# Optimization experiments

Hardware: AMD Instinct MI355X
Metric: run time of the kernel (lower is better)

The kernel has to match this reference:

```python
import jax, jax.numpy as jnp
import numpy as np

# Static config (matches init_kwargs)
B, H, W, C = 16, 64, 64, 512
HEADS, WS, SHIFT = 16, 8, 4
N = WS * WS                      # tokens per window = 64
NW = (H // WS) * (W // WS)       # windows per image = 64
HID = 4 * C                      # MLP hidden = 2048
HEAD_DIM = C // HEADS
SCALE = HEAD_DIM ** -0.5
EPS = 1e-5


def _layer_norm(x, w, b):
    m = jnp.mean(x, axis=-1, keepdims=True)
    v = jnp.mean((x - m) ** 2, axis=-1, keepdims=True)
    return (x - m) / jnp.sqrt(v + EPS) * w + b


def _rel_pos_idx():
    coords = np.stack(np.meshgrid(np.arange(WS), np.arange(WS), indexing='ij')).reshape(2, -1)
    rel = coords[:, :, None] - coords[:, None, :]          # (2, N, N)
    rel = rel.transpose(1, 2, 0)                           # (N, N, 2)
    rel[:, :, 0] += WS - 1
    rel[:, :, 1] += WS - 1
    rel[:, :, 0] *= 2 * WS - 1
    return rel.sum(-1)                                     # (N, N) int


def _attn_mask():
    img = np.zeros((H, W), dtype=np.float32)
    sls = (slice(0, -WS), slice(-WS, -SHIFT), slice(-SHIFT, None))
    cnt = 0
    for hs in sls:
        for ws_ in sls:
            img[hs, ws_] = cnt
            cnt += 1
    # window partition (H,W) -> (NW, N)
    mw = img.reshape(H // WS, WS, W // WS, WS).transpose(0, 2, 1, 3).reshape(-1, N)
    diff = mw[:, None, :] - mw[:, :, None]                 # (NW, N, N)
    return np.where(diff != 0, -100.0, 0.0).astype(np.float32)


def setup_inputs() -> dict:
    key = jax.random.key(0)
    ks = jax.random.split(key, 8)
    s = 0.02
    return {
        'x': jax.random.normal(ks[0], (B, H * W, C), jnp.float32),
        'qkv_w': jax.random.normal(ks[1], (3 * C, C), jnp.float32) * s,
        'qkv_b': jnp.zeros((3 * C,), jnp.float32),
        'proj_w': jax.random.normal(ks[2], (C, C), jnp.float32) * s,
        'proj_b': jnp.zeros((C,), jnp.float32),
        'norm1_w': jnp.ones((C,), jnp.float32),
        'norm1_b': jnp.zeros((C,), jnp.float32),
        'norm2_w': jnp.ones((C,), jnp.float32),
        'norm2_b': jnp.zeros((C,), jnp.float32),
        'fc1_w': jax.random.normal(ks[3], (HID, C), jnp.float32) * s,
        'fc1_b': jnp.zeros((HID,), jnp.float32),
        'fc2_w': jax.random.normal(ks[4], (C, HID), jnp.float32) * s,
        'fc2_b': jnp.zeros((C,), jnp.float32),
        'rel_bias_table': jax.random.normal(ks[5], ((2 * WS - 1) ** 2, HEADS), jnp.float32) * s,
        'rel_pos_idx': jnp.asarray(_rel_pos_idx(), jnp.int32),
        'attn_mask': jnp.asarray(_attn_mask(), jnp.float32),
    }


def _swin_block(x, qkv_w, qkv_b, proj_w, proj_b, norm1_w, norm1_b,
                norm2_w, norm2_b, fc1_w, fc1_b, fc2_w, fc2_b,
                rel_bias_table, rel_pos_idx, attn_mask):
    Bx = x.shape[0]
    shortcut = x
    h = _layer_norm(x, norm1_w, norm1_b).reshape(Bx, H, W, C)
    h = jnp.roll(h, (-SHIFT, -SHIFT), axis=(1, 2))
    # window partition -> (B*NW, N, C)
    h = h.reshape(Bx, H // WS, WS, W // WS, WS, C).transpose(0, 1, 3, 2, 4, 5)
    h = h.reshape(Bx * NW, N, C)
    # qkv projection
    qkv = h @ qkv_w.T + qkv_b                               # (B_, N, 3C)
    qkv = qkv.reshape(Bx * NW, N, 3, HEADS, HEAD_DIM).transpose(2, 0, 3, 1, 4)
    q, k, v = qkv[0], qkv[1], qkv[2]                        # (B_, heads, N, hd)
    attn = jnp.einsum('bhnd,bhmd->bhnm', q, k) * SCALE      # (B_, heads, N, N)
    rp_bias = rel_bias_table[rel_pos_idx]                   # (N, N, heads)
    attn = attn + rp_bias.transpose(2, 0, 1)[None]
    # shift mask (per window)
    attn = attn.reshape(Bx, NW, HEADS, N, N) + attn_mask[None, :, None]
    attn = jax.nn.softmax(attn.reshape(Bx * NW, HEADS, N, N), axis=-1)
    o = jnp.einsum('bhnm,bhmd->bhnd', attn, v)              # (B_, heads, N, hd)
    o = o.transpose(0, 2, 1, 3).reshape(Bx * NW, N, C)
    o = o @ proj_w.T + proj_b
    # window reverse -> (B, H, W, C)
    o = o.reshape(Bx, H // WS, W // WS, WS, WS, C).transpose(0, 1, 3, 2, 4, 5)
    o = o.reshape(Bx, H, W, C)
    o = jnp.roll(o, (SHIFT, SHIFT), axis=(1, 2))
    x = shortcut + o.reshape(Bx, H * W, C)
    # MLP
    h2 = _layer_norm(x, norm2_w, norm2_b)
    h2 = jax.nn.gelu(h2 @ fc1_w.T + fc1_b, approximate=False)
    return x + (h2 @ fc2_w.T + fc2_b)


def reference(x, qkv_w, qkv_b, proj_w, proj_b, norm1_w, norm1_b,
              norm2_w, norm2_b, fc1_w, fc1_b, fc2_w, fc2_b,
              rel_bias_table, rel_pos_idx, attn_mask):
    return _swin_block(x, qkv_w, qkv_b, proj_w, proj_b, norm1_w, norm1_b,
                       norm2_w, norm2_b, fc1_w, fc1_b, fc2_w, fc2_b,
                       rel_bias_table, rel_pos_idx, attn_mask)
```

## Files before the change

kernel.cpp:

```cpp
#include <hip/hip_runtime.h>
#include <hip/hip_bf16.h>

typedef __attribute__((ext_vector_type(8))) short short8;
typedef __attribute__((ext_vector_type(4))) float f32x4;

__device__ __forceinline__ short f2bfbits(float f) {
  union { __hip_bfloat16 h; short s; } cvt;
  cvt.h = __float2bfloat16(f);
  return cvt.s;
}
__device__ __forceinline__ float bfbits2f(short bits) {
  union { unsigned int u; float f; } cvt;
  cvt.u = ((unsigned int)(unsigned short)bits) << 16;
  return cvt.f;
}

__device__ __forceinline__ void gl_lds16(const short* g, short* l) {
  __builtin_amdgcn_global_load_lds(
      (__attribute__((address_space(1))) void*)(g),
      (__attribute__((address_space(3))) void*)(l), 16, 0, 0);
}

__global__ __launch_bounds__(256)
void f2bf(const float* __restrict__ s, short* __restrict__ d, int n) {
  const int i = (blockIdx.x * 256 + threadIdx.x) * 4;
  if (i >= n) return;
  float4 v = *(const float4*)(s + i);
  short o[4] = {f2bfbits(v.x), f2bfbits(v.y), f2bfbits(v.z), f2bfbits(v.w)};
  *(uint2*)(d + i) = *(const uint2*)o;
}

__global__ __launch_bounds__(256)
void bm_build(const float* __restrict__ table, const int* __restrict__ idx,
              const float* __restrict__ mask, short* __restrict__ bm) {
  const int wi = blockIdx.x, hh = blockIdx.y;
  const int n = threadIdx.x & 63;
  const int m0 = (threadIdx.x >> 6) * 16;
#pragma unroll
  for (int mm = 0; mm < 16; mm++) {
    const int m = m0 + mm;
    const float t = table[idx[m * 64 + n] * 16 + hh];
    const float mk = mask[wi * 4096 + m * 64 + n];
    bm[((long)(wi * 16 + hh) * 64 + m) * 64 + n] = f2bfbits(t + mk);
  }
}

__global__ __launch_bounds__(256)
void ln1_win(const float* __restrict__ x, const float* __restrict__ w,
             const float* __restrict__ b, short* __restrict__ h) {
  const int lane = threadIdx.x & 63;
  const int wv = threadIdx.x >> 6;
  const int t = blockIdx.x * 4 + wv;
  const int n = t & 63, wiB = t >> 6;
  const int wi = wiB & 63, bb = wiB >> 6;
  const int sr = (((wi >> 3) << 3) + (n >> 3) + 4) & 63;
  const int sc = (((wi & 7) << 3) + (n & 7) + 4) & 63;
  const float* xp = x + ((long)bb * 4096 + sr * 64 + sc) * 512 + lane * 8;
  float4 u0 = *(const float4*)(xp);
  float4 u1 = *(const float4*)(xp + 4);
  float v[8] = {u0.x, u0.y, u0.z, u0.w, u1.x, u1.y, u1.z, u1.w};
  float s = 0.f;
#pragma unroll
  for (int j = 0; j < 8; j++) s += v[j];
#pragma unroll
  for (int o = 1; o < 64; o <<= 1) s += __shfl_xor(s, o, 64);
  const float mean = s * (1.0f / 512.0f);
  float q = 0.f;
#pragma unroll
  for (int j = 0; j < 8; j++) { float d = v[j] - mean; q += d * d; }
#pragma unroll
  for (int o = 1; o < 64; o <<= 1) q += __shfl_xor(q, o, 64);
  const float rstd = rsqrtf(q * (1.0f / 512.0f) + 1e-5f);
  float4 w0 = *(const float4*)(w + lane * 8);
  float4 w1 = *(const float4*)(w + lane * 8 + 4);
  float4 b0 = *(const float4*)(b + lane * 8);
  float4 b1 = *(const float4*)(b + lane * 8 + 4);
  const float wv8[8] = {w0.x, w0.y, w0.z, w0.w, w1.x, w1.y, w1.z, w1.w};
  const float bv8[8] = {b0.x, b0.y, b0.z, b0.w, b1.x, b1.y, b1.z, b1.w};
  short outs[8];
#pragma unroll
  for (int j = 0; j < 8; j++)
    outs[j] = f2bfbits((v[j] - mean) * rstd * wv8[j] + bv8[j]);
  *(uint4*)(h + (long)t * 512 + lane * 8) = *(const uint4*)outs;
}

__global__ __launch_bounds__(256)
void ln2_id(const float* __restrict__ x2, const float* __restrict__ w,
            const float* __restrict__ b, short* __restrict__ out) {
  const int lane = threadIdx.x & 63;
  const int wv = threadIdx.x >> 6;
  const long t = blockIdx.x * 4 + wv;
  const float* xp = x2 + t * 512 + lane * 8;
  float4 u0 = *(const float4*)(xp);
  float4 u1 = *(const float4*)(xp + 4);
  float v[8] = {u0.x, u0.y, u0.z, u0.w, u1.x, u1.y, u1.z, u1.w};
  float s = 0.f;
#pragma unroll
  for (int j = 0; j < 8; j++) s += v[j];
#pragma unroll
  for (int o = 1; o < 64; o <<= 1) s += __shfl_xor(s, o, 64);
  const float mean = s * (1.0f / 512.0f);
  float q = 0.f;
#pragma unroll
  for (int j = 0; j < 8; j++) { float d = v[j] - mean; q += d * d; }
#pragma unroll
  for (int o = 1; o < 64; o <<= 1) q += __shfl_xor(q, o, 64);
  const float rstd = rsqrtf(q * (1.0f / 512.0f) + 1e-5f);
  float4 w0 = *(const float4*)(w + lane * 8);
  float4 w1 = *(const float4*)(w + lane * 8 + 4);
  float4 b0 = *(const float4*)(b + lane * 8);
  float4 b1 = *(const float4*)(b + lane * 8 + 4);
  const float wv8[8] = {w0.x, w0.y, w0.z, w0.w, w1.x, w1.y, w1.z, w1.w};
  const float bv8[8] = {b0.x, b0.y, b0.z, b0.w, b1.x, b1.y, b1.z, b1.w};
  short outs[8];
#pragma unroll
  for (int j = 0; j < 8; j++)
    outs[j] = f2bfbits((v[j] - mean) * rstd * wv8[j] + bv8[j]);
  *(uint4*)(out + t * 512 + lane * 8) = *(const uint4*)outs;
}

template <int MODE, int K, int GN>
__global__ __launch_bounds__(256, 2)
void gemm128(const short* __restrict__ A, const short* __restrict__ Bw,
             const float* __restrict__ bias, const float* __restrict__ aux,
             void* __restrict__ outv, short* __restrict__ out2) {
  __shared__ short lds[32768];
  constexpr int NT = K / 64;
  const int tid = threadIdx.x;
  const int lane = tid & 63, wave = tid >> 6;
  const int l15 = lane & 15, quad = lane >> 4;
  const int wr = wave >> 1, wc = wave & 1;

  const int nwg = gridDim.x;
  const int chunk = nwg >> 3;
  const int wg = (blockIdx.x & 7) * chunk + (blockIdx.x >> 3);
  const int row0 = (wg / GN) * 128;
  const int col0 = (wg % GN) * 128;

  const int srow = lane >> 3;
  const int scol = ((lane & 7) ^ srow) * 8;
  const short* Ag = A + (long)(row0 + wave * 32 + srow) * K + scol;
  const short* Bg = Bw + (long)(col0 + wave * 32 + srow) * K + scol;
  short* ldsAw = lds + wave * 2048;
  short* ldsBw = lds + 16384 + wave * 2048;

  const int g0 = (quad ^ (l15 & 7)) * 8;
  const int g1 = ((quad ^ 4) ^ (l15 & 7)) * 8;
  const int aB0 = (wr * 64 + l15) * 64 + g0;
  const int aB1 = (wr * 64 + l15) * 64 + g1;
  const int bB0 = 16384 + (wc * 64 + l15) * 64 + g0;
  const int bB1 = 16384 + (wc * 64 + l15) * 64 + g1;

  f32x4 acc[4][4];
#pragma unroll
  for (int m = 0; m < 4; m++)
#pragma unroll
    for (int n = 0; n < 4; n++) acc[m][n] = (f32x4){0.f, 0.f, 0.f, 0.f};

#define STAGE(cOff, kt)                                               \
  {                                                                   \
    const short* a_ = Ag + (kt) * 64;                                 \
    const short* b_ = Bg + (kt) * 64;                                 \
    _Pragma("unroll") for (int i_ = 0; i_ < 4; i_++) {                \
      gl_lds16(a_ + (long)i_ * 8 * K, ldsAw + (cOff) + i_ * 512);     \
      gl_lds16(b_ + (long)i_ * 8 * K, ldsBw + (cOff) + i_ * 512);     \
    }                                                                 \
  }

  STAGE(0, 0);
  STAGE(8192, 1);
  asm volatile("s_waitcnt vmcnt(8)" ::: "memory");
  __builtin_amdgcn_s_barrier();

  for (int t = 0; t < NT; ++t) {
    const int c = (t & 1) << 13;
    const short* pa0 = lds + c + aB0;
    const short* pa1 = lds + c + aB1;
    const short* pb0 = lds + c + bB0;
    const short* pb1 = lds + c + bB1;
    short8 A0[4], A1[4], B0[4], B1[4];

#pragma unroll
    for (int n = 0; n < 4; n++) B0[n] = *(const short8*)(pb0 + n * 1024);
#pragma unroll
    for (int m = 0; m < 4; m++) A0[m] = *(const short8*)(pa0 + m * 1024);
    asm volatile("" ::: "memory");
    __builtin_amdgcn_s_barrier();
    __builtin_amdgcn_s_setprio(1);
#pragma unroll
    for (int m = 0; m < 4; m++)
#pragma unroll
      for (int n = 0; n < 4; n++)
        acc[m][n] = __builtin_amdgcn_mfma_f32_16x16x32_bf16(A0[m], B0[n], acc[m][n], 0, 0, 0);
    __builtin_amdgcn_s_setprio(0);
    __builtin_amdgcn_s_barrier();

#pragma unroll
    for (int m = 0; m < 4; m++) A1[m] = *(const short8*)(pa1 + m * 1024);
#pragma unroll
    for (int n = 0; n < 4; n++) B1[n] = *(const short8*)(pb1 + n * 1024);
    asm volatile("s_waitcnt lgkmcnt(0)" ::: "memory");
    __builtin_amdgcn_s_barrier();
    if (t + 2 < NT) STAGE(c, t + 2);
    __builtin_amdgcn_s_setprio(1);
#pragma unroll
    for (int m = 0; m < 4; m++)
#pragma unroll
      for (int n = 0; n < 4; n++)
        acc[m][n] = __builtin_amdgcn_mfma_f32_16x16x32_bf16(A1[m], B1[n], acc[m][n], 0, 0, 0);
    __builtin_amdgcn_s_setprio(0);
    if (t + 2 < NT) {
      asm volatile("s_waitcnt vmcnt(8)" ::: "memory");
    } else if (t + 1 < NT) {
      asm volatile("s_waitcnt vmcnt(0)" ::: "memory");
    }
    __builtin_amdgcn_s_barrier();
  }
#undef STAGE

  const int rW = row0 + wr * 64;
  const int cW = col0 + wc * 64;
  if constexpr (MODE == 0) {
    if (col0 >= 1024) {
#pragma unroll
      for (int m = 0; m < 4; m++) {
        const int rbase = rW + m * 16 + quad * 4;
        const int w_ = rbase >> 6, tokb = rbase & 63;
#pragma unroll
        for (int n = 0; n < 4; n++) {
          const int col = cW + n * 16 + l15;
          const float bv = bias[col];
          const int cg = col - 1024;
          const int head = cg >> 5, d = cg & 31;
          short pk[4];
#pragma unroll
          for (int r = 0; r < 4; r++) pk[r] = f2bfbits(acc[m][n][r] + bv);
          *(uint2*)(out2 + ((long)(w_ * 16 + head) * 32 + d) * 64 + tokb) =
              *(const uint2*)pk;
        }
      }
    } else {
#pragma unroll
      for (int m = 0; m < 4; m++)
#pragma unroll
        for (int n = 0; n < 4; n++) {
          const int col = cW + n * 16 + l15;
          const float bv = bias[col];
#pragma unroll
          for (int r = 0; r < 4; r++) {
            const int row = rW + m * 16 + quad * 4 + r;
            ((short*)outv)[(long)row * 1024 + col] = f2bfbits(acc[m][n][r] + bv);
          }
        }
    }
  } else {
#pragma unroll
    for (int m = 0; m < 4; m++)
#pragma unroll
      for (int n = 0; n < 4; n++) {
        const int col = cW + n * 16 + l15;
        const float bv = bias[col];
#pragma unroll
        for (int r = 0; r < 4; r++) {
          const int row = rW + m * 16 + quad * 4 + r;
          float v = acc[m][n][r] + bv;
          if constexpr (MODE == 1) {
            const int n_ = row & 63, wiB = row >> 6;
            const int wi = wiB & 63, bb = wiB >> 6;
            const int p = (((wi >> 3) << 3) + (n_ >> 3) + 4) & 63;
            const int qq = (((wi & 7) << 3) + (n_ & 7) + 4) & 63;
            const long dst = ((long)bb * 4096 + p * 64 + qq) * 512 + col;
            ((float*)outv)[dst] = v + aux[dst];
          } else if constexpr (MODE == 2) {
            const float g = 0.5f * v * (1.0f + erff(v * 0.70710678118654752f));
            ((short*)outv)[(long)row * (GN * 128) + col] = f2bfbits(g);
          } else {
            const long ix = (long)row * (GN * 128) + col;
            ((float*)outv)[ix] = v + aux[ix];
          }
        }
      }
  }
}

__global__ __launch_bounds__(256)
void attn(const short* __restrict__ qk, const short* __restrict__ vT,
          const short* __restrict__ bm, short* __restrict__ o) {
  __shared__ short P[4][64 * 72];
  const int lane = threadIdx.x & 63, wave = threadIdx.x >> 6;
  const int l15 = lane & 15, quad = lane >> 4;
  const int w = blockIdx.x;
  const int hh = blockIdx.y * 4 + wave;
  const int wi = w & 63;
  const short* base = qk + (long)w * 64 * 1024;

  short8 qf[4], kf[4];
#pragma unroll
  for (int mt = 0; mt < 4; mt++) {
    const int tq = mt * 16 + l15;
    qf[mt] = *(const short8*)(base + tq * 1024 + hh * 32 + quad * 8);
    kf[mt] = *(const short8*)(base + tq * 1024 + 512 + hh * 32 + quad * 8);
  }
  f32x4 S[4][4];
#pragma unroll
  for (int i = 0; i < 4; i++)
#pragma unroll
    for (int j = 0; j < 4; j++) S[i][j] = (f32x4){0.f, 0.f, 0.f, 0.f};
#pragma unroll
  for (int mt = 0; mt < 4; mt++)
#pragma unroll
    for (int nt = 0; nt < 4; nt++)
      S[mt][nt] = __builtin_amdgcn_mfma_f32_16x16x32_bf16(qf[mt], kf[nt], S[mt][nt], 0, 0, 0);

  short* pw = P[wave];
  const short* bmp = bm + (long)(wi * 16 + hh) * 4096;
  const float scale = 0.17677669529663687f;
#pragma unroll
  for (int mt = 0; mt < 4; mt++) {
#pragma unroll
    for (int reg = 0; reg < 4; reg++) {
      const int m = mt * 16 + quad * 4 + reg;
      float vals[4];
#pragma unroll
      for (int nt = 0; nt < 4; nt++)
        vals[nt] = S[mt][nt][reg] * scale + bfbits2f(bmp[m * 64 + nt * 16 + l15]);
      float mx = fmaxf(fmaxf(vals[0], vals[1]), fmaxf(vals[2], vals[3]));
#pragma unroll
      for (int o_ = 1; o_ < 16; o_ <<= 1) mx = fmaxf(mx, __shfl_xor(mx, o_, 64));
      float e[4], sum = 0.f;
#pragma unroll
      for (int nt = 0; nt < 4; nt++) { e[nt] = __expf(vals[nt] - mx); sum += e[nt]; }
#pragma unroll
      for (int o_ = 1; o_ < 16; o_ <<= 1) sum += __shfl_xor(sum, o_, 64);
      const float inv = 1.0f / sum;
#pragma unroll
      for (int nt = 0; nt < 4; nt++)
        pw[m * 72 + nt * 16 + l15] = f2bfbits(e[nt] * inv);
    }
  }

  const short* vbase = vT + (long)(w * 16 + hh) * 2048;
  f32x4 O[4][2];
#pragma unroll
  for (int i = 0; i < 4; i++)
#pragma unroll
    for (int j = 0; j < 2; j++) O[i][j] = (f32x4){0.f, 0.f, 0.f, 0.f};
#pragma unroll
  for (int ks = 0; ks < 2; ks++) {
    short8 vf[2];
#pragma unroll
    for (int nt = 0; nt < 2; nt++)
      vf[nt] = *(const short8*)(vbase + (nt * 16 + l15) * 64 + ks * 32 + quad * 8);
#pragma unroll
    for (int mt = 0; mt < 4; mt++) {
      short8 pf = *(const short8*)(pw + (mt * 16 + l15) * 72 + ks * 32 + quad * 8);
#pragma unroll
      for (int nt = 0; nt < 2; nt++)
        O[mt][nt] = __builtin_amdgcn_mfma_f32_16x16x32_bf16(pf, vf[nt], O[mt][nt], 0, 0, 0);
    }
  }
#pragma unroll
  for (int mt = 0; mt < 4; mt++)
#pragma unroll
    for (int nt = 0; nt < 2; nt++)
#pragma unroll
      for (int reg = 0; reg < 4; reg++) {
        const int t = mt * 16 + quad * 4 + reg;
        const int d = nt * 16 + l15;
        o[((long)w * 64 + t) * 512 + hh * 32 + d] = f2bfbits(O[mt][nt][reg]);
      }
}

extern "C" void kernel_launch(void* const* d_in, const int* in_sizes, int n_in,
                              void* d_out, int out_size, void* d_ws, size_t ws_size,
                              hipStream_t stream) {
  const float* x      = (const float*)d_in[0];
  const float* qkv_w  = (const float*)d_in[1];
  const float* qkv_b  = (const float*)d_in[2];
  const float* proj_w = (const float*)d_in[3];
  const float* proj_b = (const float*)d_in[4];
  const float* n1w    = (const float*)d_in[5];
  const float* n1b    = (const float*)d_in[6];
  const float* n2w    = (const float*)d_in[7];
  const float* n2b    = (const float*)d_in[8];
  const float* fc1_w  = (const float*)d_in[9];
  const float* fc1_b  = (const float*)d_in[10];
  const float* fc2_w  = (const float*)d_in[11];
  const float* fc2_b  = (const float*)d_in[12];
  const float* table  = (const float*)d_in[13];
  const int*   idx    = (const int*)d_in[14];
  const float* mask   = (const float*)d_in[15];

  char* ws = (char*)d_ws;
  const long MB = 1048576L;
  short* wq  = (short*)(ws);
  short* wp  = wq + 786432;
  short* w1  = wp + 262144;
  short* w2  = w1 + 1048576;
  short* bm  = (short*)(ws + 8 * MB);
  short* h   = (short*)(ws + 17 * MB);
  short* o   = h;
  short* xn2 = h;
  short* qk  = (short*)(ws + 81 * MB);
  short* h2c = qk;
  short* vT  = (short*)(ws + 209 * MB);
  float* out = (float*)d_out;

  f2bf<<<768, 256, 0, stream>>>(qkv_w, wq, 786432);
  f2bf<<<256, 256, 0, stream>>>(proj_w, wp, 262144);
  f2bf<<<1024, 256, 0, stream>>>(fc1_w, w1, 1048576);
  f2bf<<<1024, 256, 0, stream>>>(fc2_w, w2, 1048576);
  bm_build<<<dim3(64, 16), 256, 0, stream>>>(table, idx, mask, bm);

  ln1_win<<<16384, 256, 0, stream>>>(x, n1w, n1b, h);
  gemm128<0, 512, 12><<<6144, 256, 0, stream>>>(h, wq, qkv_b, nullptr, qk, vT);
  attn<<<dim3(1024, 4), 256, 0, stream>>>(qk, vT, bm, o);
  gemm128<1, 512, 4><<<2048, 256, 0, stream>>>(o, wp, proj_b, x, out, nullptr);
  ln2_id<<<16384, 256, 0, stream>>>(out, n2w, n2b, xn2);
  for (int c = 0; c < 2; c++) {
    const long ro = (long)c * 32768;
    gemm128<2, 512, 16><<<4096, 256, 0, stream>>>(
        xn2 + ro * 512, w1, fc1_b, nullptr, h2c, nullptr);
    gemm128<3, 2048, 4><<<1024, 256, 0, stream>>>(
        h2c, w2, fc2_b, out + ro * 512, out + ro * 512, nullptr);
  }
}
```

Baseline: 991.1 us.

## Halve GEMM K-tile to 32 and raise occupancy to four blocks per CU

Shrinks the per-stage K tile of the bf16 MFMA GEMM from 64 to 32, which halves the shared-memory buffer. That lets launch bounds request four workgroups per CU instead of two. The global-to-LDS staging layout is rewritten into 8-row blocks grouped by k, so each fragment read is a contiguous 128-byte run and the XOR swizzle is no longer needed. The inner loop becomes a single MFMA phase per tile. The goal is better latency hiding through higher occupancy, paid for with twice as many loop iterations and barriers per unit of work and a tighter register budget.

```diff
diff --git a/kernel.cpp b/kernel.cpp
--- a/kernel.cpp
+++ b/kernel.cpp
@@ -120,12 +120,12 @@
 }
 
 template <int MODE, int K, int GN>
-__global__ __launch_bounds__(256, 2)
+__global__ __launch_bounds__(256, 4)
 void gemm128(const short* __restrict__ A, const short* __restrict__ Bw,
              const float* __restrict__ bias, const float* __restrict__ aux,
              void* __restrict__ outv, short* __restrict__ out2) {
-  __shared__ short lds[32768];
-  constexpr int NT = K / 64;
+  __shared__ short lds[16384];
+  constexpr int NT = K / 32;
   const int tid = threadIdx.x;
   const int lane = tid & 63, wave = tid >> 6;
   const int l15 = lane & 15, quad = lane >> 4;
@@ -137,19 +137,15 @@
   const int row0 = (wg / GN) * 128;
   const int col0 = (wg % GN) * 128;
 
-  const int srow = lane >> 3;
-  const int scol = ((lane & 7) ^ srow) * 8;
-  const short* Ag = A + (long)(row0 + wave * 32 + srow) * K + scol;
-  const short* Bg = Bw + (long)(col0 + wave * 32 + srow) * K + scol;
-  short* ldsAw = lds + wave * 2048;
-  short* ldsBw = lds + 16384 + wave * 2048;
-
-  const int g0 = (quad ^ (l15 & 7)) * 8;
-  const int g1 = ((quad ^ 4) ^ (l15 & 7)) * 8;
-  const int aB0 = (wr * 64 + l15) * 64 + g0;
-  const int aB1 = (wr * 64 + l15) * 64 + g1;
-  const int bB0 = 16384 + (wc * 64 + l15) * 64 + g0;
-  const int bB1 = 16384 + (wc * 64 + l15) * 64 + g1;
+  const int srow = ((lane >> 5) << 3) + (lane & 7);
+  const int skg = (lane >> 3) & 3;
+  const short* Ag = A + (long)(row0 + wave * 32 + srow) * K + skg * 8;
+  const short* Bg = Bw + (long)(col0 + wave * 32 + srow) * K + skg * 8;
+  short* ldsAw = lds + wave * 1024;
+  short* ldsBw = lds + 4096 + wave * 1024;
+
+  const int aOff = (wr * 8 + (l15 >> 3)) * 256 + quad * 64 + (l15 & 7) * 8;
+  const int bOff = 4096 + (wc * 8 + (l15 >> 3)) * 256 + quad * 64 + (l15 & 7) * 8;
 
   f32x4 acc[4][4];
 #pragma unroll
@@ -159,46 +155,26 @@
 
 #define STAGE(cOff, kt)                                               \
   {                                                                   \
-    const short* a_ = Ag + (kt) * 64;                                 \
-    const short* b_ = Bg + (kt) * 64;                                 \
-    _Pragma("unroll") for (int i_ = 0; i_ < 4; i_++) {                \
-      gl_lds16(a_ + (long)i_ * 8 * K, ldsAw + (cOff) + i_ * 512);     \
-      gl_lds16(b_ + (long)i_ * 8 * K, ldsBw + (cOff) + i_ * 512);     \
+    const short* a_ = Ag + (kt) * 32;                                 \
+    const short* b_ = Bg + (kt) * 32;                                 \
+    _Pragma("unroll") for (int i_ = 0; i_ < 2; i_++) {                \
+      gl_lds16(a_ + (long)i_ * 16 * K, ldsAw + (cOff) + i_ * 512);    \
+      gl_lds16(b_ + (long)i_ * 16 * K, ldsBw + (cOff) + i_ * 512);    \
     }                                                                 \
   }
 
   STAGE(0, 0);
   STAGE(8192, 1);
-  asm volatile("s_waitcnt vmcnt(8)" ::: "memory");
+  asm volatile("s_waitcnt vmcnt(4)" ::: "memory");
   __builtin_amdgcn_s_barrier();
 
   for (int t = 0; t < NT; ++t) {
     const int c = (t & 1) << 13;
-    const short* pa0 = lds + c + aB0;
-    const short* pa1 = lds + c + aB1;
-    const short* pb0 = lds + c + bB0;
-    const short* pb1 = lds + c + bB1;
-    short8 A0[4], A1[4], B0[4], B1[4];
-
-#pragma unroll
-    for (int n = 0; n < 4; n++) B0[n] = *(const short8*)(pb0 + n * 1024);
-#pragma unroll
-    for (int m = 0; m < 4; m++) A0[m] = *(const short8*)(pa0 + m * 1024);
-    asm volatile("" ::: "memory");
-    __builtin_amdgcn_s_barrier();
-    __builtin_amdgcn_s_setprio(1);
-#pragma unroll
-    for (int m = 0; m < 4; m++)
-#pragma unroll
-      for (int n = 0; n < 4; n++)
-        acc[m][n] = __builtin_amdgcn_mfma_f32_16x16x32_bf16(A0[m], B0[n], acc[m][n], 0, 0, 0);
-    __builtin_amdgcn_s_setprio(0);
-    __builtin_amdgcn_s_barrier();
-
-#pragma unroll
-    for (int m = 0; m < 4; m++) A1[m] = *(const short8*)(pa1 + m * 1024);
-#pragma unroll
-    for (int n = 0; n < 4; n++) B1[n] = *(const short8*)(pb1 + n * 1024);
+    short8 Af[4], Bf[4];
+#pragma unroll
+    for (int n = 0; n < 4; n++) Bf[n] = *(const short8*)(lds + c + bOff + n * 512);
+#pragma unroll
+    for (int m = 0; m < 4; m++) Af[m] = *(const short8*)(lds + c + aOff + m * 512);
     asm volatile("s_waitcnt lgkmcnt(0)" ::: "memory");
     __builtin_amdgcn_s_barrier();
     if (t + 2 < NT) STAGE(c, t + 2);
@@ -207,10 +183,10 @@
     for (int m = 0; m < 4; m++)
 #pragma unroll
       for (int n = 0; n < 4; n++)
-        acc[m][n] = __builtin_amdgcn_mfma_f32_16x16x32_bf16(A1[m], B1[n], acc[m][n], 0, 0, 0);
+        acc[m][n] = __builtin_amdgcn_mfma_f32_16x16x32_bf16(Af[m], Bf[n], acc[m][n], 0, 0, 0);
     __builtin_amdgcn_s_setprio(0);
     if (t + 2 < NT) {
-      asm volatile("s_waitcnt vmcnt(8)" ::: "memory");
+      asm volatile("s_waitcnt vmcnt(4)" ::: "memory");
     } else if (t + 1 < NT) {
       asm volatile("s_waitcnt vmcnt(0)" ::: "memory");
     }
```

Result: slower. 1.230 ms (+24.1%).
